# Performance work log

Measured on AMD Instinct MI355X. Metric: run time of the kernel, lower is better.

## Reference

```python
import jax, jax.numpy as jnp
import numpy as np

BASE = 10000.0

def _rope_neox(x, positions, head_dim):
    # x: [B, S, n_heads, head_dim]; positions: [B, S] int
    half = head_dim // 2
    inv_freq = 1.0 / (BASE ** (jnp.arange(0, head_dim, 2, dtype=jnp.float32) / head_dim))  # [half]
    freqs = positions.astype(jnp.float32)[..., None] * inv_freq  # [B, S, half]
    cos = jnp.cos(freqs)[:, :, None, :]  # [B, S, 1, half]
    sin = jnp.sin(freqs)[:, :, None, :]
    x1, x2 = x[..., :half], x[..., half:]
    return jnp.concatenate([x1 * cos - x2 * sin, x2 * cos + x1 * sin], axis=-1)

def setup_inputs() -> dict:
    key = jax.random.key(0)
    k1, k2, k3 = jax.random.split(key, 3)
    B, S, H = 1, 2048, 4096
    hidden_states = jax.random.normal(k1, (B, S, H), dtype=jnp.float32)
    position_ids = jnp.broadcast_to(jnp.arange(S, dtype=jnp.int32), (B, S))
    W_qkv = jax.random.normal(k2, (H, 3 * H), dtype=jnp.float32) * (H ** -0.5)
    W_o = jax.random.normal(k3, (H, H), dtype=jnp.float32) * (H ** -0.5)
    return {"hidden_states": hidden_states, "position_ids": position_ids, "W_qkv": W_qkv, "W_o": W_o}

def reference(hidden_states, position_ids, W_qkv, W_o):
    B, S, H = hidden_states.shape
    n_heads = 32
    head_dim = H // n_heads
    qkv = hidden_states @ W_qkv  # [B, S, 3H]
    q, k, v = jnp.split(qkv, 3, axis=-1)
    q = q.reshape(B, S, n_heads, head_dim)
    k = k.reshape(B, S, n_heads, head_dim)
    v = v.reshape(B, S, n_heads, head_dim)
    q = _rope_neox(q, position_ids, head_dim)
    k = _rope_neox(k, position_ids, head_dim)
    # causal SDPA (past_key_value=None -> is_causal=True)
    scale = 1.0 / jnp.sqrt(jnp.float32(head_dim))
    scores = jnp.einsum('bqhd,bkhd->bhqk', q, k) * scale  # [B, nH, S, S]
    causal = jnp.tril(jnp.ones((S, S), dtype=bool))
    scores = jnp.where(causal, scores, jnp.finfo(scores.dtype).min)
    probs = jax.nn.softmax(scores, axis=-1)
    attn = jnp.einsum('bhqk,bkhd->bqhd', probs, v).reshape(B, S, H)
    return attn @ W_o
```

## Files before the change

### kernel.cpp

```cpp
#include <hip/hip_runtime.h>
#include <hip/hip_bf16.h>
#include <math.h>

#define SEQ   2048
#define HID   4096
#define NHEAD 32
#define HD    128
#define QKVN  12288

typedef __bf16 bf16;
typedef __bf16 bf16x8 __attribute__((ext_vector_type(8)));
typedef __bf16 bf16x4 __attribute__((ext_vector_type(4)));
typedef float  f32x4  __attribute__((ext_vector_type(4)));

#define AS1 __attribute__((address_space(1)))
#define AS3 __attribute__((address_space(3)))

__device__ __forceinline__ void gload16(const void* g, void* l) {
    __builtin_amdgcn_global_load_lds((const AS1 void*)g, (AS3 void*)l, 16, 0, 0);
}

__device__ __forceinline__ unsigned short bbits(bf16 b) {
    union { bf16 b; unsigned short u; } x; x.b = b; return x.u;
}

template<int OB>
__global__ __launch_bounds__(256) void gemm_bt(const bf16* __restrict__ A,
                                               const bf16* __restrict__ Bt,
                                               void* __restrict__ Cv,
                                               int M, int N, int K) {
    __shared__ __attribute__((aligned(16))) char smem[32768];
    const int tid  = threadIdx.x;
    const int l    = tid & 63;
    const int wave = tid >> 6;
    const int wr   = wave >> 1, wc = wave & 1;
    const int brow = blockIdx.y * 128, bcol = blockIdx.x * 128;

    f32x4 acc[4][4];
    #pragma unroll
    for (int i = 0; i < 4; ++i)
        #pragma unroll
        for (int j = 0; j < 4; ++j) acc[i][j] = (f32x4){0.f, 0.f, 0.f, 0.f};

    const size_t rowb = (size_t)K * 2;
    const char* gA[2]; const char* gB[2]; int ldsOff[2];
    #pragma unroll
    for (int i = 0; i < 2; ++i) {
        int c  = i * 256 + tid;
        int r  = c >> 2, sl = c & 3;
        int so = (sl * 16) ^ ((r & 3) << 4);
        gA[i] = (const char*)A + (size_t)(brow + r) * rowb + so;
        gB[i] = (const char*)Bt + (size_t)(bcol + r) * rowb + so;
        ldsOff[i] = (i * 256 + (tid & 192)) * 16;
    }

    int afo[4], bfo[4];
    #pragma unroll
    for (int f = 0; f < 4; ++f) {
        int ra = wr * 64 + f * 16 + (l & 15);
        int rb = wc * 64 + f * 16 + (l & 15);
        int sw = (((l >> 4) * 16) ^ ((l & 3) << 4));
        afo[f] = ra * 64 + sw;
        bfo[f] = rb * 64 + sw;
    }

#define STAGE(buf) do { \
        gload16(gA[0], smem + (buf) * 8192 + ldsOff[0]); \
        gload16(gA[1], smem + (buf) * 8192 + ldsOff[1]); \
        gload16(gB[0], smem + 16384 + (buf) * 8192 + ldsOff[0]); \
        gload16(gB[1], smem + 16384 + (buf) * 8192 + ldsOff[1]); \
        gA[0] += 64; gA[1] += 64; gB[0] += 64; gB[1] += 64; \
    } while (0)

#define COMPUTE(buf) do { \
        const char* Ab_ = smem + (buf) * 8192; \
        const char* Bb_ = smem + 16384 + (buf) * 8192; \
        bf16x8 af[4], bfr[4]; \
        _Pragma("unroll") \
        for (int f = 0; f < 4; ++f) { \
            af[f]  = *(const bf16x8*)(Ab_ + afo[f]); \
            bfr[f] = *(const bf16x8*)(Bb_ + bfo[f]); \
        } \
        _Pragma("unroll") \
        for (int mf = 0; mf < 4; ++mf) \
            _Pragma("unroll") \
            for (int nf = 0; nf < 4; ++nf) \
                acc[mf][nf] = __builtin_amdgcn_mfma_f32_16x16x32_bf16(af[mf], bfr[nf], acc[mf][nf], 0, 0, 0); \
    } while (0)

    const int NT = K >> 5;
    STAGE(0);
    asm volatile("s_waitcnt vmcnt(0)" ::: "memory");
    __builtin_amdgcn_s_barrier();
    for (int t = 0; t < NT - 1; ++t) {
        const int cur = t & 1;
        STAGE(cur ^ 1);
        COMPUTE(cur);
        asm volatile("s_waitcnt vmcnt(0) lgkmcnt(0)" ::: "memory");
        __builtin_amdgcn_s_barrier();
    }
    COMPUTE((NT - 1) & 1);
#undef STAGE
#undef COMPUTE

    __syncthreads();
    float* ep = (float*)smem + wave * (16 * 68);
    #pragma unroll
    for (int mf = 0; mf < 4; ++mf) {
        #pragma unroll
        for (int nf = 0; nf < 4; ++nf)
            #pragma unroll
            for (int j = 0; j < 4; ++j)
                ep[((l >> 4) * 4 + j) * 68 + nf * 16 + (l & 15)] = acc[mf][nf][j];
        if (OB == 0) {
            #pragma unroll
            for (int p = 0; p < 4; ++p) {
                int row = p * 4 + (l >> 4);
                f32x4 v = *(const f32x4*)(ep + row * 68 + (l & 15) * 4);
                size_t grow = (size_t)(brow + wr * 64 + mf * 16 + row);
                *(f32x4*)((float*)Cv + grow * N + bcol + wc * 64 + (l & 15) * 4) = v;
            }
        } else {
            #pragma unroll
            for (int p = 0; p < 2; ++p) {
                int row = p * 8 + (l >> 3);
                const float* src = ep + row * 68 + (l & 7) * 8;
                bf16x8 o;
                #pragma unroll
                for (int i = 0; i < 8; ++i) o[i] = (bf16)src[i];
                size_t grow = (size_t)(brow + wr * 64 + mf * 16 + row);
                *(bf16x8*)((bf16*)Cv + grow * N + bcol + wc * 64 + (l & 7) * 8) = o;
            }
        }
    }
}

__global__ __launch_bounds__(256) void cast_flat(const float* __restrict__ in,
                                                 bf16* __restrict__ out, int n8) {
    int i = blockIdx.x * 256 + threadIdx.x;
    if (i >= n8) return;
    float4 a = ((const float4*)in)[2 * i];
    float4 b = ((const float4*)in)[2 * i + 1];
    bf16x8 o = {(bf16)a.x, (bf16)a.y, (bf16)a.z, (bf16)a.w,
                (bf16)b.x, (bf16)b.y, (bf16)b.z, (bf16)b.w};
    *(bf16x8*)(out + (size_t)i * 8) = o;
}

__global__ __launch_bounds__(256) void cast_transpose(const float* __restrict__ in,
                                                      bf16* __restrict__ out, int R, int C) {
    __shared__ float t[64][65];
    const int r0 = blockIdx.y * 64, c0 = blockIdx.x * 64;
    #pragma unroll
    for (int i = 0; i < 4; ++i) {
        int idx = i * 256 + threadIdx.x;
        int rr = idx >> 4, c4 = (idx & 15) * 4;
        float4 v = *(const float4*)&in[(size_t)(r0 + rr) * C + c0 + c4];
        t[rr][c4] = v.x; t[rr][c4 + 1] = v.y; t[rr][c4 + 2] = v.z; t[rr][c4 + 3] = v.w;
    }
    __syncthreads();
    #pragma unroll
    for (int i = 0; i < 2; ++i) {
        int idx = i * 256 + threadIdx.x;
        int rr = idx >> 3, c8 = (idx & 7) * 8;
        bf16x8 o;
        #pragma unroll
        for (int j = 0; j < 8; ++j) o[j] = (bf16)t[c8 + j][rr];
        *(bf16x8*)&out[(size_t)(c0 + rr) * R + r0 + c8] = o;
    }
}

__global__ __launch_bounds__(256) void rope_table(const int* __restrict__ pos_ids,
                                                  float2* __restrict__ tab) {
    int id = blockIdx.x * 256 + threadIdx.x;
    int s = id >> 6, d = id & 63;
    float pos = (float)pos_ids[s];
    float inv = expf(-9.210340371976184f * ((float)d * (1.0f / 64.0f)));
    float sn, cs;
    sincosf(pos * inv, &sn, &cs);
    tab[id] = make_float2(cs, sn);
}

__global__ __launch_bounds__(256) void rope_repack(const bf16* __restrict__ qkv,
                                                   const float2* __restrict__ tab,
                                                   bf16* __restrict__ Qb,
                                                   bf16* __restrict__ Kb) {
    int id = blockIdx.x * 256 + threadIdx.x;
    const int d4 = (id & 15) * 4;
    const int h  = (id >> 4) & (NHEAD - 1);
    const int s  = id >> 9;

    float2 tr[4];
    #pragma unroll
    for (int i = 0; i < 4; ++i) tr[i] = tab[s * 64 + d4 + i];

    const bf16* row = qkv + (size_t)s * QKVN;
    {
        bf16x4 lo = *(const bf16x4*)(row + h * HD + d4);
        bf16x4 hi = *(const bf16x4*)(row + h * HD + 64 + d4);
        bf16x4 olo, ohi;
        #pragma unroll
        for (int i = 0; i < 4; ++i) {
            float x1 = (float)lo[i], x2 = (float)hi[i];
            olo[i] = (bf16)(x1 * tr[i].x - x2 * tr[i].y);
            ohi[i] = (bf16)(x2 * tr[i].x + x1 * tr[i].y);
        }
        bf16* qo = Qb + ((size_t)h * SEQ + s) * HD;
        *(bf16x4*)(qo + d4) = olo;
        *(bf16x4*)(qo + 64 + d4) = ohi;
    }
    {
        bf16x4 lo = *(const bf16x4*)(row + HID + h * HD + d4);
        bf16x4 hi = *(const bf16x4*)(row + HID + h * HD + 64 + d4);
        bf16x4 olo, ohi;
        #pragma unroll
        for (int i = 0; i < 4; ++i) {
            float x1 = (float)lo[i], x2 = (float)hi[i];
            olo[i] = (bf16)(x1 * tr[i].x - x2 * tr[i].y);
            ohi[i] = (bf16)(x2 * tr[i].x + x1 * tr[i].y);
        }
        bf16* ko = Kb + ((size_t)h * SEQ + s) * HD;
        *(bf16x4*)(ko + d4) = olo;
        *(bf16x4*)(ko + 64 + d4) = ohi;
    }
}

__global__ __launch_bounds__(256) void v_transpose(const bf16* __restrict__ qkv,
                                                   bf16* __restrict__ Vt) {
    __shared__ bf16 t[64][130];
    const int h = blockIdx.y, s0 = blockIdx.x * 64;
    #pragma unroll
    for (int i = 0; i < 4; ++i) {
        int idx = i * 256 + threadIdx.x;
        int ss = idx >> 4, c8 = (idx & 15) * 8;
        bf16x8 v = *(const bf16x8*)&qkv[(size_t)(s0 + ss) * QKVN + 2 * HID + h * HD + c8];
        #pragma unroll
        for (int j = 0; j < 8; ++j) t[ss][c8 + j] = v[j];
    }
    __syncthreads();
    #pragma unroll
    for (int i = 0; i < 4; ++i) {
        int idx = i * 256 + threadIdx.x;
        int dd = idx >> 3, s8 = (idx & 7) * 8;
        bf16x8 o;
        #pragma unroll
        for (int j = 0; j < 8; ++j) o[j] = t[s8 + j][dd];
        *(bf16x8*)&Vt[((size_t)h * HD + dd) * SEQ + s0 + s8] = o;
    }
}

__global__ __launch_bounds__(256) void attn_mfma(const bf16* __restrict__ Qb,
                                                 const bf16* __restrict__ Kb,
                                                 const bf16* __restrict__ Vt,
                                                 bf16* __restrict__ attn) {
    __shared__ __attribute__((aligned(16))) char Ka[2][16384];
    __shared__ __attribute__((aligned(16))) char Va[2][16384];
    __shared__ __attribute__((aligned(16))) char Ps[4 * 2048];
    const int tid  = threadIdx.x, l = tid & 63, wave = tid >> 6;
    const int head = blockIdx.x;
    const int qb   = gridDim.y - 1 - blockIdx.y;
    const int q0   = qb * 64;
    const int qw   = q0 + wave * 16;
    const float scale = 0.08838834764831845f;

    bf16x8 qf[4];
    const bf16* Qg = Qb + ((size_t)head * SEQ + qw + (l & 15)) * HD;
    #pragma unroll
    for (int kc = 0; kc < 4; ++kc) qf[kc] = *(const bf16x8*)(Qg + kc * 32 + (l >> 4) * 8);

    f32x4 o[8];
    #pragma unroll
    for (int i = 0; i < 8; ++i) o[i] = (f32x4){0.f, 0.f, 0.f, 0.f};
    float mrun = -1e30f, lrun = 0.f;
    const int qrow  = qw + (l & 15);
    const int ntile = qb + 1;

    const char* Kg = (const char*)(Kb + (size_t)head * SEQ * HD);
    const char* Vg = (const char*)(Vt + (size_t)head * HD * SEQ);
    char* Pw = Ps + wave * 2048;

#define ASTAGE(b, t0) do { \
        const int kv0_ = (t0) * 64; \
        _Pragma("unroll") \
        for (int i = 0; i < 4; ++i) { \
            int c = i * 256 + tid; \
            int rk_ = c >> 4, slk_ = c & 15; \
            gload16(Kg + (size_t)(kv0_ + rk_) * 256 + ((slk_ * 16) ^ ((rk_ & 15) << 4)), \
                    Ka[b] + (size_t)(i * 256 + (tid & 192)) * 16); \
            int rv_ = c >> 3, slv_ = c & 7; \
            gload16(Vg + (size_t)rv_ * (SEQ * 2) + (size_t)kv0_ * 2 + ((slv_ * 16) ^ ((rv_ & 7) << 4)), \
                    Va[b] + (size_t)(i * 256 + (tid & 192)) * 16); \
        } \
    } while (0)

    ASTAGE(0, 0);
    asm volatile("s_waitcnt vmcnt(0)" ::: "memory");
    __builtin_amdgcn_s_barrier();

    for (int t = 0; t < ntile; ++t) {
        const int cur = t & 1;
        const int kv0 = t * 64;
        if (t + 1 < ntile) ASTAGE(cur ^ 1, t + 1);

        f32x4 st[4];
        __builtin_amdgcn_s_setprio(1);
        #pragma unroll
        for (int mf = 0; mf < 4; ++mf) {
            f32x4 s = (f32x4){0.f, 0.f, 0.f, 0.f};
            #pragma unroll
            for (int kc = 0; kc < 4; ++kc) {
                int rk = mf * 16 + (l & 15);
                bf16x8 a = *(const bf16x8*)(Ka[cur] + rk * 256 +
                              ((kc * 64 + (l >> 4) * 16) ^ ((rk & 15) << 4)));
                s = __builtin_amdgcn_mfma_f32_16x16x32_bf16(a, qf[kc], s, 0, 0, 0);
            }
            st[mf] = s;
        }
        __builtin_amdgcn_s_setprio(0);

        float pm = -1e30f;
        #pragma unroll
        for (int mf = 0; mf < 4; ++mf)
            #pragma unroll
            for (int j = 0; j < 4; ++j) {
                int kv = kv0 + mf * 16 + (l >> 4) * 4 + j;
                float v = (kv <= qrow) ? st[mf][j] * scale : -1e30f;
                st[mf][j] = v;
                pm = fmaxf(pm, v);
            }
        pm = fmaxf(pm, __shfl_xor(pm, 16));
        pm = fmaxf(pm, __shfl_xor(pm, 32));
        float mn   = fmaxf(mrun, pm);
        float corr = __expf(mrun - mn);
        float ls = 0.f;
        #pragma unroll
        for (int mf = 0; mf < 4; ++mf)
            #pragma unroll
            for (int j = 0; j < 4; ++j) {
                float p = __expf(st[mf][j] - mn);
                st[mf][j] = p;
                ls += p;
            }
        ls += __shfl_xor(ls, 16);
        ls += __shfl_xor(ls, 32);
        lrun = lrun * corr + ls;
        mrun = mn;

        f32x4 cv;
        #pragma unroll
        for (int r = 0; r < 4; ++r) cv[r] = __shfl(corr, (l >> 4) * 4 + r, 64);
        #pragma unroll
        for (int nf = 0; nf < 8; ++nf) o[nf] *= cv;

        #pragma unroll
        for (int mf = 0; mf < 4; ++mf)
            #pragma unroll
            for (int r = 0; r < 4; r += 2) {
                int kv = mf * 16 + (l >> 4) * 4 + r;
                unsigned pk = (unsigned)bbits((bf16)st[mf][r]) |
                              ((unsigned)bbits((bf16)st[mf][r + 1]) << 16);
                *(unsigned*)(Pw + (l & 15) * 128 + ((kv * 2) ^ ((l & 15 & 7) << 4))) = pk;
            }

        __builtin_amdgcn_s_setprio(1);
        #pragma unroll
        for (int kc = 0; kc < 2; ++kc) {
            bf16x8 pa = *(const bf16x8*)(Pw + (l & 15) * 128 +
                           ((kc * 64 + (l >> 4) * 16) ^ ((l & 7) << 4)));
            #pragma unroll
            for (int nf = 0; nf < 8; ++nf) {
                int dr = nf * 16 + (l & 15);
                bf16x8 vb = *(const bf16x8*)(Va[cur] + dr * 128 +
                               ((kc * 64 + (l >> 4) * 16) ^ ((dr & 7) << 4)));
                o[nf] = __builtin_amdgcn_mfma_f32_16x16x32_bf16(pa, vb, o[nf], 0, 0, 0);
            }
        }
        __builtin_amdgcn_s_setprio(0);

        asm volatile("s_waitcnt vmcnt(0) lgkmcnt(0)" ::: "memory");
        __builtin_amdgcn_s_barrier();
    }
#undef ASTAGE

    float il = 1.0f / lrun;
    f32x4 iv;
    #pragma unroll
    for (int r = 0; r < 4; ++r) iv[r] = __shfl(il, (l >> 4) * 4 + r, 64);
    #pragma unroll
    for (int nf = 0; nf < 8; ++nf)
        #pragma unroll
        for (int r = 0; r < 4; ++r) {
            int row = qw + (l >> 4) * 4 + r;
            attn[(size_t)row * HID + head * HD + nf * 16 + (l & 15)] = (bf16)(o[nf][r] * iv[r]);
        }
}

extern "C" void kernel_launch(void* const* d_in, const int* in_sizes, int n_in,
                              void* d_out, int out_size, void* d_ws, size_t ws_size,
                              hipStream_t stream) {
    const float* hidden  = (const float*)d_in[0];
    const int*   pos_ids = (const int*)d_in[1];
    const float* W_qkv   = (const float*)d_in[2];
    const float* W_o     = (const float*)d_in[3];
    float*       out     = (float*)d_out;
    char*        ws      = (char*)d_ws;

    bf16*   Wqkv_t   = (bf16*)(ws);
    bf16*   qkv_b    = (bf16*)(ws + 100663296);
    bf16*   hidden_b = (bf16*)(ws + 150994944);
    float2* tab      = (float2*)(ws + 150994944);
    bf16* Qb     = (bf16*)(ws);
    bf16* Kb     = (bf16*)(ws + 16777216);
    bf16* Vtb    = (bf16*)(ws + 33554432);
    bf16* attn_b = (bf16*)(ws + 50331648);
    bf16* Wo_t   = (bf16*)(ws + 67108864);

    cast_flat<<<SEQ * HID / 8 / 256, 256, 0, stream>>>(hidden, hidden_b, SEQ * HID / 8);
    cast_transpose<<<dim3(QKVN / 64, HID / 64), 256, 0, stream>>>(W_qkv, Wqkv_t, HID, QKVN);
    gemm_bt<1><<<dim3(QKVN / 128, SEQ / 128), 256, 0, stream>>>(hidden_b, Wqkv_t, qkv_b,
                                                                SEQ, QKVN, HID);
    rope_table<<<SEQ * 64 / 256, 256, 0, stream>>>(pos_ids, tab);
    rope_repack<<<SEQ * NHEAD * 16 / 256, 256, 0, stream>>>(qkv_b, tab, Qb, Kb);
    v_transpose<<<dim3(SEQ / 64, NHEAD), 256, 0, stream>>>(qkv_b, Vtb);
    cast_transpose<<<dim3(HID / 64, HID / 64), 256, 0, stream>>>(W_o, Wo_t, HID, HID);
    attn_mfma<<<dim3(NHEAD, SEQ / 64), 256, 0, stream>>>(Qb, Kb, Vtb, attn_b);
    gemm_bt<0><<<dim3(HID / 128, SEQ / 128), 256, 0, stream>>>(attn_b, Wo_t, out,
                                                               SEQ, HID, HID);
}
```

Baseline: 523.7 us.

## Add 256x256-tile 8-wave GEMM with double-buffered async LDS loads for QKV projection

Introduces a new bf16 GEMM kernel using 256x256 output tiles, 512 threads and 128 KB of LDS. Global-to-LDS loads are split into quarter-tile stages interleaved with MFMA phases, with s_setprio raising priority around the MFMA blocks. It replaces the 128x128 GEMM for the large QKV projection to raise arithmetic intensity and overlap memory with compute. The cost is lower occupancy and fewer blocks (48x8), which may leave some CUs underused or unevenly loaded.

```diff
diff --git a/kernel.cpp b/kernel.cpp
--- a/kernel.cpp
+++ b/kernel.cpp
@@ -22,6 +22,139 @@
 
 __device__ __forceinline__ unsigned short bbits(bf16 b) {
     union { bf16 b; unsigned short u; } x; x.b = b; return x.u;
+}
+
+__global__ __launch_bounds__(512) void gemm256_bt(const bf16* __restrict__ A,
+                                                  const bf16* __restrict__ Bt,
+                                                  bf16* __restrict__ C,
+                                                  int M, int N, int K) {
+    __shared__ __attribute__((aligned(16))) char lds[131072];
+    const int tid  = threadIdx.x;
+    const int l    = tid & 63;
+    const int wave = tid >> 6;
+    const int wr   = wave >> 2;
+    const int wc   = wave & 3;
+    const int lh   = l >> 4;
+    const int ll   = l & 15;
+    const int brow = blockIdx.y * 256, bcol = blockIdx.x * 256;
+
+    f32x4 acc[4][4][2];
+    #pragma unroll
+    for (int q = 0; q < 4; ++q)
+        #pragma unroll
+        for (int f = 0; f < 4; ++f)
+            #pragma unroll
+            for (int g = 0; g < 2; ++g) acc[q][f][g] = (f32x4){0.f, 0.f, 0.f, 0.f};
+
+    const int trow = tid >> 3, tslot = tid & 7;
+    const int srcs = (tslot ^ (trow & 7)) * 16;
+    const size_t rowb = (size_t)K * 2;
+    const char* pA[2][2]; const char* pB[2][2];
+    #pragma unroll
+    for (int h = 0; h < 2; ++h)
+        #pragma unroll
+        for (int i = 0; i < 2; ++i) {
+            pA[h][i] = (const char*)A  + (size_t)(brow + h*128 + i*64 + trow) * rowb + srcs;
+            pB[h][i] = (const char*)Bt + (size_t)(bcol + h*128 + i*64 + trow) * rowb + srcs;
+        }
+
+#define SA(buf, h) do { \
+        gload16(pA[h][0], lds + (buf)*65536 + (h)*16384 + tid*16); \
+        gload16(pA[h][1], lds + (buf)*65536 + (h)*16384 + 8192 + tid*16); \
+        pA[h][0] += 128; pA[h][1] += 128; \
+    } while (0)
+#define SB(buf, h) do { \
+        gload16(pB[h][0], lds + (buf)*65536 + 32768 + (h)*16384 + tid*16); \
+        gload16(pB[h][1], lds + (buf)*65536 + 32768 + (h)*16384 + 8192 + tid*16); \
+        pB[h][0] += 128; pB[h][1] += 128; \
+    } while (0)
+
+    const int sw0 = ((0 + lh) ^ (ll & 7)) << 4;
+    const int sw1 = ((4 + lh) ^ (ll & 7)) << 4;
+
+#define PHASE(Xb, mh, nh, STAGE_STMT, WAITSTR) do { \
+        const char* LA_ = lds + (Xb)*65536 + (mh)*16384 + (wr*64 + ll)*128; \
+        const char* LB_ = lds + (Xb)*65536 + 32768 + (nh)*16384 + (wc*32 + ll)*128; \
+        bf16x8 af_[4][2], bv_[2][2]; \
+        _Pragma("unroll") \
+        for (int f_ = 0; f_ < 4; ++f_) { \
+            af_[f_][0] = *(const bf16x8*)(LA_ + f_*2048 + sw0); \
+            af_[f_][1] = *(const bf16x8*)(LA_ + f_*2048 + sw1); \
+        } \
+        _Pragma("unroll") \
+        for (int g_ = 0; g_ < 2; ++g_) { \
+            bv_[g_][0] = *(const bf16x8*)(LB_ + g_*2048 + sw0); \
+            bv_[g_][1] = *(const bf16x8*)(LB_ + g_*2048 + sw1); \
+        } \
+        STAGE_STMT; \
+        asm volatile(WAITSTR ::: "memory"); \
+        __builtin_amdgcn_s_barrier(); \
+        asm volatile("s_waitcnt lgkmcnt(0)" ::: "memory"); \
+        __builtin_amdgcn_s_setprio(1); \
+        _Pragma("unroll") \
+        for (int f_ = 0; f_ < 4; ++f_) \
+            _Pragma("unroll") \
+            for (int g_ = 0; g_ < 2; ++g_) { \
+                acc[(mh)*2+(nh)][f_][g_] = __builtin_amdgcn_mfma_f32_16x16x32_bf16( \
+                    af_[f_][0], bv_[g_][0], acc[(mh)*2+(nh)][f_][g_], 0, 0, 0); \
+                acc[(mh)*2+(nh)][f_][g_] = __builtin_amdgcn_mfma_f32_16x16x32_bf16( \
+                    af_[f_][1], bv_[g_][1], acc[(mh)*2+(nh)][f_][g_], 0, 0, 0); \
+            } \
+        __builtin_amdgcn_s_setprio(0); \
+        __builtin_amdgcn_s_barrier(); \
+    } while (0)
+
+    SA(0, 0); SB(0, 0); SB(0, 1); SA(0, 1); SA(1, 0); SB(1, 0);
+    asm volatile("s_waitcnt vmcnt(8)" ::: "memory");
+    __builtin_amdgcn_s_barrier();
+
+    const int NT = K >> 6;
+    for (int u = 0; u < NT - 1; ++u) {
+        const int X = u & 1, Y = X ^ 1;
+        PHASE(X, 0, 0, SB(Y, 1), "s_waitcnt vmcnt(8)");
+        PHASE(X, 0, 1, SA(Y, 1), "s_waitcnt vmcnt(8)");
+        if (u < NT - 2) {
+            PHASE(X, 1, 0, SA(X, 0), "s_waitcnt vmcnt(8)");
+            PHASE(X, 1, 1, SB(X, 0), "s_waitcnt vmcnt(8)");
+        } else {
+            PHASE(X, 1, 0, ((void)0), "s_waitcnt vmcnt(8)");
+            PHASE(X, 1, 1, ((void)0), "s_waitcnt vmcnt(8)");
+        }
+    }
+    {
+        const int X = (NT - 1) & 1;
+        PHASE(X, 0, 0, ((void)0), "s_waitcnt vmcnt(4)");
+        PHASE(X, 0, 1, ((void)0), "s_waitcnt vmcnt(2)");
+        PHASE(X, 1, 0, ((void)0), "s_waitcnt vmcnt(0)");
+        PHASE(X, 1, 1, ((void)0), "s_nop 0");
+    }
+#undef PHASE
+#undef SA
+#undef SB
+
+    float* ep = (float*)lds + wave * 2304;
+    const int c8 = (l & 3) * 8;
+    #pragma unroll
+    for (int q = 0; q < 4; ++q) {
+        const int mh = q >> 1, nh = q & 1;
+        #pragma unroll
+        for (int f = 0; f < 4; ++f)
+            #pragma unroll
+            for (int g = 0; g < 2; ++g)
+                #pragma unroll
+                for (int j = 0; j < 4; ++j)
+                    ep[(f*16 + lh*4 + j) * 36 + g*16 + ll] = acc[q][f][g][j];
+        #pragma unroll
+        for (int it = 0; it < 4; ++it) {
+            int r2 = it * 16 + (l >> 2);
+            const float* src = ep + r2 * 36 + c8;
+            bf16x8 o;
+            #pragma unroll
+            for (int j = 0; j < 8; ++j) o[j] = (bf16)src[j];
+            size_t grow = (size_t)(brow + mh*128 + wr*64 + r2);
+            *(bf16x8*)(C + grow * N + bcol + nh*128 + wc*32 + c8) = o;
+        }
+    }
 }
 
 template<int OB>
@@ -416,7 +549,7 @@
 
     cast_flat<<<SEQ * HID / 8 / 256, 256, 0, stream>>>(hidden, hidden_b, SEQ * HID / 8);
     cast_transpose<<<dim3(QKVN / 64, HID / 64), 256, 0, stream>>>(W_qkv, Wqkv_t, HID, QKVN);
-    gemm_bt<1><<<dim3(QKVN / 128, SEQ / 128), 256, 0, stream>>>(hidden_b, Wqkv_t, qkv_b,
+    gemm256_bt<<<dim3(QKVN / 256, SEQ / 256), 512, 0, stream>>>(hidden_b, Wqkv_t, qkv_b,
                                                                 SEQ, QKVN, HID);
     rope_table<<<SEQ * 64 / 256, 256, 0, stream>>>(pos_ids, tab);
     rope_repack<<<SEQ * NHEAD * 16 / 256, 256, 0, stream>>>(qkv_b, tab, Qb, Kb);
```

Result: slower. 957.5 us (+82.8%).

## Rewrite GEMM as 256x128 tile, 8-wave ping-pong kernel with XCD-aware scheduling

Applied to the files above, without the earlier changes.

Replaces the 128x128, 4-wave GEMM with a 512-thread kernel that computes 256x128 tiles with a K-step of 64. It splits each K-step into two phases, one per M-half, and interleaves global-to-LDS loads for the next buffer with MFMA work, using s_setprio and barriers. Block IDs are remapped so neighbouring tiles land on the same XCD for better L2 reuse. The kernel uses 96KB of LDS and bounds of two blocks per CU, and the hand-tuned vmcnt waits and XOR swizzle add correctness risk.

```diff
diff --git a/kernel.cpp b/kernel.cpp
--- a/kernel.cpp
+++ b/kernel.cpp
@@ -25,111 +25,145 @@
 }
 
 template<int OB>
-__global__ __launch_bounds__(256) void gemm_bt(const bf16* __restrict__ A,
-                                               const bf16* __restrict__ Bt,
-                                               void* __restrict__ Cv,
-                                               int M, int N, int K) {
-    __shared__ __attribute__((aligned(16))) char smem[32768];
+__global__ __launch_bounds__(512, 2) void gemm2p(const bf16* __restrict__ A,
+                                                 const bf16* __restrict__ Bt,
+                                                 void* __restrict__ Cv,
+                                                 int M, int N, int K, int gx) {
+    __shared__ __attribute__((aligned(16))) char lds[98304];
     const int tid  = threadIdx.x;
     const int l    = tid & 63;
     const int wave = tid >> 6;
-    const int wr   = wave >> 1, wc = wave & 1;
-    const int brow = blockIdx.y * 128, bcol = blockIdx.x * 128;
-
-    f32x4 acc[4][4];
-    #pragma unroll
-    for (int i = 0; i < 4; ++i)
-        #pragma unroll
-        for (int j = 0; j < 4; ++j) acc[i][j] = (f32x4){0.f, 0.f, 0.f, 0.f};
-
+    const int wr   = wave >> 2;
+    const int wc   = wave & 3;
+    const int lh   = l >> 4;
+    const int ll   = l & 15;
+
+    const int id   = blockIdx.x;
+    const int xcd  = id & 7;
+    const int slot = id >> 3;
+    const int bx   = xcd * (gx >> 3) + (slot >> 3);
+    const int by   = slot & 7;
+    const int brow = by * 256, bcol = bx * 128;
+
+    f32x4 acc[2][4][2];
+    #pragma unroll
+    for (int m = 0; m < 2; ++m)
+        #pragma unroll
+        for (int f = 0; f < 4; ++f)
+            #pragma unroll
+            for (int g = 0; g < 2; ++g) acc[m][f][g] = (f32x4){0.f, 0.f, 0.f, 0.f};
+
+    const int trow = tid >> 3, tslot = tid & 7;
+    const int srcs = (tslot ^ (trow & 7)) * 16;
     const size_t rowb = (size_t)K * 2;
-    const char* gA[2]; const char* gB[2]; int ldsOff[2];
-    #pragma unroll
-    for (int i = 0; i < 2; ++i) {
-        int c  = i * 256 + tid;
-        int r  = c >> 2, sl = c & 3;
-        int so = (sl * 16) ^ ((r & 3) << 4);
-        gA[i] = (const char*)A + (size_t)(brow + r) * rowb + so;
-        gB[i] = (const char*)Bt + (size_t)(bcol + r) * rowb + so;
-        ldsOff[i] = (i * 256 + (tid & 192)) * 16;
-    }
-
-    int afo[4], bfo[4];
-    #pragma unroll
-    for (int f = 0; f < 4; ++f) {
-        int ra = wr * 64 + f * 16 + (l & 15);
-        int rb = wc * 64 + f * 16 + (l & 15);
-        int sw = (((l >> 4) * 16) ^ ((l & 3) << 4));
-        afo[f] = ra * 64 + sw;
-        bfo[f] = rb * 64 + sw;
-    }
-
-#define STAGE(buf) do { \
-        gload16(gA[0], smem + (buf) * 8192 + ldsOff[0]); \
-        gload16(gA[1], smem + (buf) * 8192 + ldsOff[1]); \
-        gload16(gB[0], smem + 16384 + (buf) * 8192 + ldsOff[0]); \
-        gload16(gB[1], smem + 16384 + (buf) * 8192 + ldsOff[1]); \
-        gA[0] += 64; gA[1] += 64; gB[0] += 64; gB[1] += 64; \
+    const char* pA[2][2]; const char* pB[2];
+    #pragma unroll
+    for (int h = 0; h < 2; ++h)
+        #pragma unroll
+        for (int i = 0; i < 2; ++i)
+            pA[h][i] = (const char*)A + (size_t)(brow + h*128 + i*64 + trow) * rowb + srcs;
+    #pragma unroll
+    for (int i = 0; i < 2; ++i)
+        pB[i] = (const char*)Bt + (size_t)(bcol + i*64 + trow) * rowb + srcs;
+
+#define SA(buf, h) do { \
+        gload16(pA[h][0], lds + (buf)*32768 + (h)*16384 + tid*16); \
+        gload16(pA[h][1], lds + (buf)*32768 + (h)*16384 + 8192 + tid*16); \
+        pA[h][0] += 128; pA[h][1] += 128; \
     } while (0)
-
-#define COMPUTE(buf) do { \
-        const char* Ab_ = smem + (buf) * 8192; \
-        const char* Bb_ = smem + 16384 + (buf) * 8192; \
-        bf16x8 af[4], bfr[4]; \
+#define SB(buf) do { \
+        gload16(pB[0], lds + 65536 + (buf)*16384 + tid*16); \
+        gload16(pB[1], lds + 65536 + (buf)*16384 + 8192 + tid*16); \
+        pB[0] += 128; pB[1] += 128; \
+    } while (0)
+
+    const int sw0 = ((0 + lh) ^ (ll & 7)) << 4;
+    const int sw1 = ((4 + lh) ^ (ll & 7)) << 4;
+
+#define PHASE(Xb, mh, STAGE_STMT, WAITSTR) do { \
+        const char* LA_ = lds + (Xb)*32768 + (mh)*16384 + (wr*64 + ll)*128; \
+        const char* LB_ = lds + 65536 + (Xb)*16384 + (wc*32 + ll)*128; \
+        bf16x8 af_[4][2], bv_[2][2]; \
         _Pragma("unroll") \
-        for (int f = 0; f < 4; ++f) { \
-            af[f]  = *(const bf16x8*)(Ab_ + afo[f]); \
-            bfr[f] = *(const bf16x8*)(Bb_ + bfo[f]); \
+        for (int f_ = 0; f_ < 4; ++f_) { \
+            af_[f_][0] = *(const bf16x8*)(LA_ + f_*2048 + sw0); \
+            af_[f_][1] = *(const bf16x8*)(LA_ + f_*2048 + sw1); \
         } \
         _Pragma("unroll") \
-        for (int mf = 0; mf < 4; ++mf) \
+        for (int g_ = 0; g_ < 2; ++g_) { \
+            bv_[g_][0] = *(const bf16x8*)(LB_ + g_*2048 + sw0); \
+            bv_[g_][1] = *(const bf16x8*)(LB_ + g_*2048 + sw1); \
+        } \
+        STAGE_STMT; \
+        asm volatile(WAITSTR ::: "memory"); \
+        __builtin_amdgcn_s_barrier(); \
+        asm volatile("s_waitcnt lgkmcnt(0)" ::: "memory"); \
+        __builtin_amdgcn_sched_barrier(0); \
+        __builtin_amdgcn_s_setprio(1); \
+        _Pragma("unroll") \
+        for (int f_ = 0; f_ < 4; ++f_) \
             _Pragma("unroll") \
-            for (int nf = 0; nf < 4; ++nf) \
-                acc[mf][nf] = __builtin_amdgcn_mfma_f32_16x16x32_bf16(af[mf], bfr[nf], acc[mf][nf], 0, 0, 0); \
+            for (int g_ = 0; g_ < 2; ++g_) { \
+                acc[mh][f_][g_] = __builtin_amdgcn_mfma_f32_16x16x32_bf16( \
+                    af_[f_][0], bv_[g_][0], acc[mh][f_][g_], 0, 0, 0); \
+                acc[mh][f_][g_] = __builtin_amdgcn_mfma_f32_16x16x32_bf16( \
+                    af_[f_][1], bv_[g_][1], acc[mh][f_][g_], 0, 0, 0); \
+            } \
+        __builtin_amdgcn_s_setprio(0); \
+        __builtin_amdgcn_s_barrier(); \
     } while (0)
 
-    const int NT = K >> 5;
-    STAGE(0);
-    asm volatile("s_waitcnt vmcnt(0)" ::: "memory");
+    SA(0, 0); SB(0); SA(0, 1); SA(1, 0);
+    asm volatile("s_waitcnt vmcnt(4)" ::: "memory");
     __builtin_amdgcn_s_barrier();
-    for (int t = 0; t < NT - 1; ++t) {
-        const int cur = t & 1;
-        STAGE(cur ^ 1);
-        COMPUTE(cur);
-        asm volatile("s_waitcnt vmcnt(0) lgkmcnt(0)" ::: "memory");
-        __builtin_amdgcn_s_barrier();
-    }
-    COMPUTE((NT - 1) & 1);
-#undef STAGE
-#undef COMPUTE
+
+    const int NT = K >> 6;
+    for (int u = 0; u < NT - 2; ++u) {
+        const int X = u & 1, Y = X ^ 1;
+        PHASE(X, 0, SB(Y), "s_waitcnt vmcnt(4)");
+        PHASE(X, 1, { SA(Y, 1); SA(X, 0); }, "s_waitcnt vmcnt(4)");
+    }
+    {
+        const int X = (NT - 2) & 1, Y = X ^ 1;
+        PHASE(X, 0, SB(Y), "s_waitcnt vmcnt(4)");
+        PHASE(X, 1, SA(Y, 1), "s_waitcnt vmcnt(2)");
+    }
+    {
+        const int X = (NT - 1) & 1;
+        PHASE(X, 0, ((void)0), "s_waitcnt vmcnt(0)");
+        PHASE(X, 1, ((void)0), "s_nop 0");
+    }
+#undef PHASE
+#undef SA
+#undef SB
 
     __syncthreads();
-    float* ep = (float*)smem + wave * (16 * 68);
-    #pragma unroll
-    for (int mf = 0; mf < 4; ++mf) {
-        #pragma unroll
-        for (int nf = 0; nf < 4; ++nf)
-            #pragma unroll
-            for (int j = 0; j < 4; ++j)
-                ep[((l >> 4) * 4 + j) * 68 + nf * 16 + (l & 15)] = acc[mf][nf][j];
-        if (OB == 0) {
-            #pragma unroll
-            for (int p = 0; p < 4; ++p) {
-                int row = p * 4 + (l >> 4);
-                f32x4 v = *(const f32x4*)(ep + row * 68 + (l & 15) * 4);
-                size_t grow = (size_t)(brow + wr * 64 + mf * 16 + row);
-                *(f32x4*)((float*)Cv + grow * N + bcol + wc * 64 + (l & 15) * 4) = v;
-            }
-        } else {
-            #pragma unroll
-            for (int p = 0; p < 2; ++p) {
-                int row = p * 8 + (l >> 3);
-                const float* src = ep + row * 68 + (l & 7) * 8;
+    float* ep = (float*)lds + wave * 2304;
+    const int cq = l & 3;
+    #pragma unroll
+    for (int mh = 0; mh < 2; ++mh) {
+        #pragma unroll
+        for (int f = 0; f < 4; ++f)
+            #pragma unroll
+            for (int g = 0; g < 2; ++g)
+                #pragma unroll
+                for (int j = 0; j < 4; ++j)
+                    ep[(f*16 + lh*4 + j) * 36 + g*16 + ll] = acc[mh][f][g][j];
+        #pragma unroll
+        for (int it = 0; it < 4; ++it) {
+            int r2 = it * 16 + (l >> 2);
+            const float* src = ep + r2 * 36 + cq * 8;
+            size_t grow = (size_t)(brow + mh*128 + wr*64 + r2);
+            int gcol = bcol + wc*32 + cq*8;
+            if (OB == 0) {
+                float* dst = (float*)Cv + grow * N + gcol;
+                *(f32x4*)dst       = *(const f32x4*)src;
+                *(f32x4*)(dst + 4) = *(const f32x4*)(src + 4);
+            } else {
                 bf16x8 o;
                 #pragma unroll
-                for (int i = 0; i < 8; ++i) o[i] = (bf16)src[i];
-                size_t grow = (size_t)(brow + wr * 64 + mf * 16 + row);
-                *(bf16x8*)((bf16*)Cv + grow * N + bcol + wc * 64 + (l & 7) * 8) = o;
+                for (int jj = 0; jj < 8; ++jj) o[jj] = (bf16)src[jj];
+                *(bf16x8*)((bf16*)Cv + grow * N + gcol) = o;
             }
         }
     }
@@ -416,13 +450,13 @@
 
     cast_flat<<<SEQ * HID / 8 / 256, 256, 0, stream>>>(hidden, hidden_b, SEQ * HID / 8);
     cast_transpose<<<dim3(QKVN / 64, HID / 64), 256, 0, stream>>>(W_qkv, Wqkv_t, HID, QKVN);
-    gemm_bt<1><<<dim3(QKVN / 128, SEQ / 128), 256, 0, stream>>>(hidden_b, Wqkv_t, qkv_b,
-                                                                SEQ, QKVN, HID);
+    gemm2p<1><<<(QKVN / 128) * (SEQ / 256), 512, 0, stream>>>(hidden_b, Wqkv_t, qkv_b,
+                                                              SEQ, QKVN, HID, QKVN / 128);
     rope_table<<<SEQ * 64 / 256, 256, 0, stream>>>(pos_ids, tab);
     rope_repack<<<SEQ * NHEAD * 16 / 256, 256, 0, stream>>>(qkv_b, tab, Qb, Kb);
     v_transpose<<<dim3(SEQ / 64, NHEAD), 256, 0, stream>>>(qkv_b, Vtb);
     cast_transpose<<<dim3(HID / 64, HID / 64), 256, 0, stream>>>(W_o, Wo_t, HID, HID);
     attn_mfma<<<dim3(NHEAD, SEQ / 64), 256, 0, stream>>>(Qb, Kb, Vtb, attn_b);
-    gemm_bt<0><<<dim3(HID / 128, SEQ / 128), 256, 0, stream>>>(attn_b, Wo_t, out,
-                                                               SEQ, HID, HID);
-}
+    gemm2p<0><<<(HID / 128) * (SEQ / 256), 512, 0, stream>>>(attn_b, Wo_t, out,
+                                                             SEQ, HID, HID, HID / 128);
+}
```

Result: faster. 463.8 us (-11.5%).
